# Performance work log

Measured on AMD Instinct MI355X. Metric: run time of the kernel, lower is better.

The kernel has to match this reference:

```python
import jax, jax.numpy as jnp
import numpy as np
import math

BLOCK = 256
NUM_HEADS = 32
HEAD_DIM = 128
HIDDEN = 2048
INNER = NUM_HEADS * HEAD_DIM
SEQ = 4096
EPS = 1e-5
LAYER_IDX = 0
NUM_LAYERS = 32


def _build_slopes(n):
    def get_slopes(n):
        def pow2(m):
            start = 2 ** (-2 ** (-(math.log2(m) - 3)))
            return [start * start ** i for i in range(m)]
        if math.log2(n).is_integer():
            return pow2(n)
        c = 2 ** math.floor(math.log2(n))
        return pow2(c) + get_slopes(2 * c)[0::2][: n - c]
    s = np.asarray(get_slopes(n), dtype=np.float32).reshape(n, 1, 1)
    # layer decay scaling as in __init__
    s = s * (1.0 - LAYER_IDX / (NUM_LAYERS - 1) + 1e-5)
    return s


def setup_inputs() -> dict:
    key = jax.random.key(0)
    k1, k2, k3, k4 = jax.random.split(key, 4)
    sd_h = 1.0 / math.sqrt(HIDDEN)
    sd_i = 1.0 / math.sqrt(INNER)
    return {
        "hidden_states": jax.random.normal(k1, (SEQ, HIDDEN), jnp.float32),
        "w_qkv": jax.random.normal(k2, (HIDDEN, 3 * INNER), jnp.float32) * sd_h,
        "w_gate": jax.random.normal(k3, (HIDDEN, INNER), jnp.float32) * sd_h,
        "w_out": jax.random.normal(k4, (INNER, HIDDEN), jnp.float32) * sd_i,
        "norm_weight": jnp.ones((INNER,), jnp.float32),
        "slope_rate": jnp.asarray(_build_slopes(NUM_HEADS)),
        "kv_cache": jnp.zeros((NUM_HEADS, HEAD_DIM, HEAD_DIM), jnp.float32),
    }


def _lightning_attention(q, k, v, slope, kv0):
    # q,k,v: [h, n, d]; slope: [h,1,1]; kv0: [h, d, d]
    h, n, d = q.shape
    nb = n // BLOCK
    qb = q.reshape(h, nb, BLOCK, d).transpose(1, 0, 2, 3)  # [nb,h,B,d]
    kb = k.reshape(h, nb, BLOCK, d).transpose(1, 0, 2, 3)
    vb = v.reshape(h, nb, BLOCK, d).transpose(1, 0, 2, 3)

    idx = jnp.arange(BLOCK, dtype=jnp.float32)
    diff = idx[:, None] - idx[None, :]                      # i - j
    s = slope.reshape(h, 1, 1)
    intra_decay = jnp.where(diff >= 0, jnp.exp(-s * diff), 0.0)   # [h,B,B]
    q_decay = jnp.exp(-s * (idx + 1.0).reshape(1, BLOCK, 1))      # [h,B,1]
    k_decay = jnp.exp(-s * (BLOCK - 1.0 - idx).reshape(1, BLOCK, 1))  # [h,B,1]
    block_decay = jnp.exp(-s * BLOCK)                             # [h,1,1]

    def step(kv, blk):
        qc, kc, vc = blk  # each [h,B,d]
        scores = jnp.einsum('hid,hjd->hij', qc, kc) * intra_decay
        o_intra = jnp.einsum('hij,hjd->hid', scores, vc)
        o_inter = q_decay * jnp.einsum('hid,hde->hie', qc, kv)
        kv_new = block_decay * kv + jnp.einsum('hjd,hje->hde', kc * k_decay, vc)
        return kv_new, o_intra + o_inter

    kv_final, outs = jax.lax.scan(step, kv0, (qb, kb, vb))
    out = outs.transpose(1, 0, 2, 3).reshape(h, n, d)
    return out, kv_final


def reference(hidden_states, w_qkv, w_gate, w_out, norm_weight, slope_rate, kv_cache):
    n = hidden_states.shape[0]
    # qkv projection + SiLU activation (done in fp32 in the original)
    qkv = jax.nn.silu(hidden_states @ w_qkv)                  # [n, 3*inner]
    qkv = qkv.reshape(n, NUM_HEADS, 3 * HEAD_DIM)
    q, k, v = jnp.split(qkv, 3, axis=-1)                      # [n,h,d] each
    q = q.transpose(1, 0, 2)                                  # [h,n,d]
    k = k.transpose(1, 0, 2)
    v = v.transpose(1, 0, 2)

    attn, kv_final = _lightning_attention(q, k, v, slope_rate, kv_cache)
    attn = attn.transpose(1, 0, 2).reshape(n, INNER)          # n (h d)

    # RMSNorm (fp32) then sigmoid gate then output projection
    var = jnp.mean(attn * attn, axis=-1, keepdims=True)
    normed = attn * jax.lax.rsqrt(var + EPS) * norm_weight
    gate = jax.nn.sigmoid(hidden_states @ w_gate)
    out = (gate * normed) @ w_out                             # [n, hidden]
    return out
```

## Files before the change

### kernel.cpp

```cpp
#include <hip/hip_runtime.h>
#include <stdint.h>

typedef __bf16 bf16x8 __attribute__((ext_vector_type(8)));
typedef float  f32x4  __attribute__((ext_vector_type(4)));
typedef unsigned short u16x8 __attribute__((ext_vector_type(8)));

__device__ __forceinline__ unsigned short f2bf(float f) {
    union { float f; uint32_t u; } x; x.f = f;
    uint32_t r = (x.u + 0x7FFFu + ((x.u >> 16) & 1u)) >> 16;
    return (unsigned short)r;
}
__device__ __forceinline__ float bf2f(unsigned short b) {
    union { uint32_t u; float f; } x; x.u = ((uint32_t)b) << 16;
    return x.f;
}

__device__ __forceinline__ void gl16(const void* g, void* l) {
    __builtin_amdgcn_global_load_lds(
        (const __attribute__((address_space(1))) void*)g,
        (__attribute__((address_space(3))) void*)(uint32_t)(uintptr_t)l,
        16, 0, 0);
}

#define MFMA16(a, b, c) __builtin_amdgcn_mfma_f32_16x16x32_bf16((a), (b), (c), 0, 0, 0)

__global__ __launch_bounds__(256) void f32_to_bf16_kernel(const float* __restrict__ in,
                                                          unsigned short* __restrict__ out,
                                                          int n8) {
    int i = blockIdx.x * 256 + threadIdx.x;
    if (i >= n8) return;
    float4 a = ((const float4*)in)[2 * i];
    float4 b = ((const float4*)in)[2 * i + 1];
    u16x8 o;
    o[0] = f2bf(a.x); o[1] = f2bf(a.y); o[2] = f2bf(a.z); o[3] = f2bf(a.w);
    o[4] = f2bf(b.x); o[5] = f2bf(b.y); o[6] = f2bf(b.z); o[7] = f2bf(b.w);
    ((u16x8*)out)[i] = o;
}

__global__ __launch_bounds__(256) void transpose_w_kernel(const float* __restrict__ in,
                                                          unsigned short* __restrict__ out,
                                                          int R, int C) {
    __shared__ float tile[32][33];
    int c0 = blockIdx.x * 32, r0 = blockIdx.y * 32;
    int lx = threadIdx.x & 31, ly = threadIdx.x >> 5;
#pragma unroll
    for (int i = ly; i < 32; i += 8)
        tile[i][lx] = in[(size_t)(r0 + i) * C + c0 + lx];
    __syncthreads();
#pragma unroll
    for (int i = ly; i < 32; i += 8)
        out[(size_t)(c0 + i) * R + r0 + lx] = f2bf(tile[lx][i]);
}

template <int ACT, int OUTF32>
__global__ __launch_bounds__(512, 2) void gemm256_kernel(const unsigned short* __restrict__ A,
                                                         const unsigned short* __restrict__ Bt,
                                                         void* __restrict__ Cout,
                                                         int N, int K, int NBN) {
    __shared__ unsigned short Abuf[2][2][8192];
    __shared__ unsigned short Bbuf[2][2][8192];

    int nwg = gridDim.x;
    int bid = blockIdx.x;
    int wg = (bid & 7) * (nwg >> 3) + (bid >> 3);
    int bm = wg / NBN, bn = wg % NBN;
    int tid = threadIdx.x, lane = tid & 63, w = tid >> 6;
    int wr = w >> 2, wc = w & 3;

    int r0 = tid >> 3;
    int cbs = (tid & 7) << 4;
    int el0 = (cbs ^ ((r0 & 7) << 4)) >> 1;
    int r1 = 64 + r0;
    int el1 = (cbs ^ ((r1 & 7) << 4)) >> 1;
    int lo0 = tid * 16, lo1 = 8192 + tid * 16;

    const unsigned short* Ag0 = A + (size_t)(bm * 256) * K;
    const unsigned short* Ag1 = A + (size_t)(bm * 256 + 128) * K;
    const unsigned short* Bg0 = Bt + (size_t)(bn * 256) * K;
    const unsigned short* Bg1 = Bt + (size_t)(bn * 256 + 128) * K;

#define STAGE(src, dstHalf, k0)                                            \
    do {                                                                   \
        gl16((src) + (size_t)r0 * K + (k0) + el0, (char*)(dstHalf) + lo0); \
        gl16((src) + (size_t)r1 * K + (k0) + el1, (char*)(dstHalf) + lo1); \
    } while (0)

    int aRow = wr * 64 + (lane & 15);
    int bRow = wc * 32 + (lane & 15);
    int swz = (lane & 7) << 4;
    int cbb = (lane >> 4) << 4;

#define RD_A(slot, R, m, kk) \
    af[R][m][kk] = *(const bf16x8*)((const char*)Abuf[slot][R] + ((aRow + (m) * 16) << 7) + (((kk) * 64 + cbb) ^ swz))
#define RD_B(slot, Cq, n, kk) \
    bfr[Cq][n][kk] = *(const bf16x8*)((const char*)Bbuf[slot][Cq] + ((bRow + (n) * 16) << 7) + (((kk) * 64 + cbb) ^ swz))

#define QUAD(q, Rh, Cc)                                                       \
    do {                                                                      \
        _Pragma("unroll")                                                     \
        for (int m = 0; m < 4; ++m)                                           \
            _Pragma("unroll")                                                 \
            for (int n = 0; n < 2; ++n) {                                     \
                acc[q][m][n] = MFMA16(af[Rh][m][0], bfr[Cc][n][0], acc[q][m][n]); \
                acc[q][m][n] = MFMA16(af[Rh][m][1], bfr[Cc][n][1], acc[q][m][n]); \
            }                                                                 \
    } while (0)

    bf16x8 af[2][4][2];
    bf16x8 bfr[2][2][2];
    f32x4 acc[4][4][2];
#pragma unroll
    for (int q = 0; q < 4; ++q)
#pragma unroll
        for (int m = 0; m < 4; ++m)
#pragma unroll
            for (int n = 0; n < 2; ++n)
#pragma unroll
                for (int r = 0; r < 4; ++r) acc[q][m][n][r] = 0.f;

    int NT = K >> 6;
    STAGE(Ag0, Abuf[0][0], 0);
    STAGE(Bg0, Bbuf[0][0], 0);
    STAGE(Ag1, Abuf[0][1], 0);
    STAGE(Bg1, Bbuf[0][1], 0);
    STAGE(Ag0, Abuf[1][0], 64);
    STAGE(Bg0, Bbuf[1][0], 64);
    STAGE(Ag1, Abuf[1][1], 64);
    STAGE(Bg1, Bbuf[1][1], 64);
    asm volatile("s_waitcnt vmcnt(8)" ::: "memory");
    __builtin_amdgcn_s_barrier();
#pragma unroll
    for (int m = 0; m < 4; ++m) { RD_A(0, 0, m, 0); RD_A(0, 0, m, 1); }
#pragma unroll
    for (int n = 0; n < 2; ++n) { RD_B(0, 0, n, 0); RD_B(0, 0, n, 1); }

    for (int t = 0; t < NT; ++t) {
        int cur = t & 1, nx = cur ^ 1;
        bool rd = (t + 1 < NT);
        bool st = (t + 2 < NT);
        int ks = (t + 2) << 6;

#pragma unroll
        for (int m = 0; m < 4; ++m) { RD_A(cur, 1, m, 0); RD_A(cur, 1, m, 1); }
        asm volatile("s_waitcnt lgkmcnt(8)" ::: "memory");
        __builtin_amdgcn_sched_barrier(0);
        __builtin_amdgcn_s_setprio(1);
        QUAD(0, 0, 0);
        __builtin_amdgcn_s_setprio(0);

#pragma unroll
        for (int n = 0; n < 2; ++n) { RD_B(cur, 1, n, 0); RD_B(cur, 1, n, 1); }
        asm volatile("s_waitcnt lgkmcnt(4)" ::: "memory");
        __builtin_amdgcn_sched_barrier(0);
        __builtin_amdgcn_s_setprio(1);
        QUAD(1, 1, 0);
        __builtin_amdgcn_s_setprio(0);

        asm volatile("s_waitcnt lgkmcnt(0)" ::: "memory");
        asm volatile("s_waitcnt vmcnt(0)" ::: "memory");
        __builtin_amdgcn_s_barrier();
        if (st) {
            STAGE(Ag0, Abuf[cur][0], ks);
            STAGE(Bg0, Bbuf[cur][0], ks);
        }
        if (rd) {
#pragma unroll
            for (int n = 0; n < 2; ++n) { RD_B(nx, 0, n, 0); RD_B(nx, 0, n, 1); }
        }
        __builtin_amdgcn_s_setprio(1);
        QUAD(2, 0, 1);
        __builtin_amdgcn_s_setprio(0);

        if (st) {
            STAGE(Ag1, Abuf[cur][1], ks);
            STAGE(Bg1, Bbuf[cur][1], ks);
        }
        if (rd) {
#pragma unroll
            for (int m = 0; m < 4; ++m) { RD_A(nx, 0, m, 0); RD_A(nx, 0, m, 1); }
        }
        __builtin_amdgcn_s_setprio(1);
        QUAD(3, 1, 1);
        __builtin_amdgcn_s_setprio(0);
    }

#pragma unroll
    for (int q = 0; q < 4; ++q) {
        const int R_ = q & 1, C_ = q >> 1;
#pragma unroll
        for (int m = 0; m < 4; ++m) {
            int row0 = bm * 256 + R_ * 128 + wr * 64 + m * 16 + ((lane >> 4) * 4);
#pragma unroll
            for (int n = 0; n < 2; ++n) {
                int col = bn * 256 + C_ * 128 + wc * 32 + n * 16 + (lane & 15);
#pragma unroll
                for (int rg = 0; rg < 4; ++rg) {
                    float v = acc[q][m][n][rg];
                    if (ACT == 1) v = v / (1.f + __expf(-v));
                    else if (ACT == 2) v = 1.f / (1.f + __expf(-v));
                    size_t idx = (size_t)(row0 + rg) * N + col;
                    if (OUTF32) ((float*)Cout)[idx] = v;
                    else        ((unsigned short*)Cout)[idx] = f2bf(v);
                }
            }
        }
    }
#undef STAGE
#undef RD_A
#undef RD_B
#undef QUAD
}

__global__ __launch_bounds__(256) void kv_transpose_kernel(const unsigned short* __restrict__ qkv,
                                                           const float* __restrict__ slopes,
                                                           unsigned short* __restrict__ kts,
                                                           unsigned short* __restrict__ vt) {
    __shared__ unsigned short tk[32][33];
    __shared__ unsigned short tv[32][33];
    int n0 = blockIdx.x * 32, d0 = blockIdx.y * 32, h = blockIdx.z;
    float s = slopes[h];
    int lx = threadIdx.x & 31, ly = threadIdx.x >> 5;
#pragma unroll
    for (int i = ly; i < 32; i += 8) {
        int n = n0 + i;
        size_t rowb = (size_t)n * 12288 + h * 384;
        float kv = bf2f(qkv[rowb + 128 + d0 + lx]) * __expf(-s * (float)(255 - (n & 255)));
        tk[i][lx] = f2bf(kv);
        tv[i][lx] = qkv[rowb + 256 + d0 + lx];
    }
    __syncthreads();
#pragma unroll
    for (int i = ly; i < 32; i += 8) {
        size_t ob = (size_t)(h * 128 + d0 + i) * 4096 + n0 + lx;
        kts[ob] = tk[lx][i];
        vt[ob] = tv[lx][i];
    }
}

__global__ __launch_bounds__(256) void kv_outer_kernel(const unsigned short* __restrict__ kts,
                                                       const unsigned short* __restrict__ vt,
                                                       float* __restrict__ U) {
    __shared__ unsigned short Kc[128 * 64];
    __shared__ unsigned short Vc[128 * 64];
    int blk = blockIdx.x;
    int h = blk & 31, t = blk >> 5;
    int tid = threadIdx.x, lane = tid & 63, w = tid >> 6;

    f32x4 acc[2][8];
#pragma unroll
    for (int m = 0; m < 2; ++m)
#pragma unroll
        for (int n = 0; n < 8; ++n)
#pragma unroll
            for (int r = 0; r < 4; ++r) acc[m][n][r] = 0.f;

    for (int ks = 0; ks < 4; ++ks) {
        __syncthreads();
#pragma unroll
        for (int it = 0; it < 4; ++it) {
            int slot = it * 256 + tid;
            int o = slot * 16;
            int r = o >> 7;
            int cb = o & 127;
            int scb = cb ^ ((r & 7) << 4);
            size_t j = (size_t)t * 256 + ks * 64 + (scb >> 1);
            gl16(kts + (size_t)(h * 128 + r) * 4096 + j, (char*)Kc + o);
            gl16(vt + (size_t)(h * 128 + r) * 4096 + j, (char*)Vc + o);
        }
        __syncthreads();
#pragma unroll
        for (int kk = 0; kk < 2; ++kk) {
            int kb = kk * 64 + ((lane >> 4) * 16);
            bf16x8 vf[2], kf[8];
#pragma unroll
            for (int m = 0; m < 2; ++m) {
                int e = w * 32 + m * 16 + (lane & 15);
                vf[m] = *(const bf16x8*)((const char*)Vc + (e << 7) + (kb ^ ((e & 7) << 4)));
            }
#pragma unroll
            for (int n = 0; n < 8; ++n) {
                int d = n * 16 + (lane & 15);
                kf[n] = *(const bf16x8*)((const char*)Kc + (d << 7) + (kb ^ ((d & 7) << 4)));
            }
#pragma unroll
            for (int m = 0; m < 2; ++m)
#pragma unroll
                for (int n = 0; n < 8; ++n)
                    acc[m][n] = MFMA16(vf[m], kf[n], acc[m][n]);
        }
    }
    size_t base = (size_t)(h * 16 + t) * 16384;
#pragma unroll
    for (int m = 0; m < 2; ++m)
#pragma unroll
        for (int n = 0; n < 8; ++n)
#pragma unroll
            for (int r = 0; r < 4; ++r) {
                int e = w * 32 + m * 16 + ((lane >> 4) * 4) + r;
                int d = n * 16 + (lane & 15);
                U[base + (size_t)e * 128 + d] = acc[m][n][r];
            }
}

__global__ __launch_bounds__(256) void kv_scan_kernel(const float* __restrict__ kv_cache,
                                                      const float* __restrict__ U,
                                                      const float* __restrict__ slopes,
                                                      unsigned short* __restrict__ Wb) {
    int h = blockIdx.x >> 3;
    int c0 = (blockIdx.x & 7) * 2048;
    int tid = threadIdx.x;
    float s = slopes[h];
    float bd = __expf(-s * 256.f);
    float wst[8];
    size_t hb = (size_t)h * 16384;
#pragma unroll
    for (int i = 0; i < 8; ++i) {
        int idx = c0 + i * 256 + tid;
        int e = idx >> 7, d = idx & 127;
        wst[i] = kv_cache[hb + (size_t)d * 128 + e];
    }
    for (int t = 0; t < 16; ++t) {
        size_t base = (size_t)(h * 16 + t) * 16384 + c0;
#pragma unroll
        for (int i = 0; i < 8; ++i) {
            int idx = i * 256 + tid;
            Wb[base + idx] = f2bf(wst[i]);
            wst[i] = bd * wst[i] + U[base + idx];
        }
    }
}

__global__ __launch_bounds__(256, 1) void attn_out_kernel(const unsigned short* __restrict__ qkv,
                                                          const unsigned short* __restrict__ vt,
                                                          const unsigned short* __restrict__ Wb,
                                                          const float* __restrict__ slopes,
                                                          unsigned short* __restrict__ attn) {
    __shared__ unsigned short lds[65536];
    unsigned short* Qs = lds;
    unsigned short* Ps = lds + 32768;
    unsigned short* KW = lds + 49152;
    unsigned short* Ks = KW;
    unsigned short* Vs = KW + 8192;

    int blk = blockIdx.x;
    int h = blk & 31, t = blk >> 5;
    float s = slopes[h];
    int tid = threadIdx.x, lane = tid & 63, w = tid >> 6;

#pragma unroll
    for (int it = 0; it < 16; ++it) {
        int slot = it * 256 + tid;
        int o = slot * 16;
        int r = o >> 8, cb = o & 255, scb = cb ^ ((r & 7) << 4);
        gl16(qkv + (size_t)(t * 256 + r) * 12288 + h * 384 + (scb >> 1), (char*)Qs + o);
    }
#pragma unroll
    for (int it = 0; it < 8; ++it) {
        int slot = it * 256 + tid;
        int o = slot * 16;
        int e = o >> 8, cb = o & 255, scb = cb ^ ((e & 7) << 4);
        gl16(Wb + (size_t)((h * 16 + t) * 128 + e) * 128 + (scb >> 1), (char*)KW + o);
    }
    __syncthreads();

    f32x4 acc[4][8];
#pragma unroll
    for (int m = 0; m < 4; ++m)
#pragma unroll
        for (int n = 0; n < 8; ++n)
#pragma unroll
            for (int r = 0; r < 4; ++r) acc[m][n][r] = 0.f;

#pragma unroll
    for (int kk = 0; kk < 4; ++kk) {
        int kb = kk * 64 + ((lane >> 4) * 16);
        bf16x8 qf[4], wf[8];
#pragma unroll
        for (int m = 0; m < 4; ++m) {
            int r = w * 64 + m * 16 + (lane & 15);
            qf[m] = *(const bf16x8*)((const char*)Qs + (r << 8) + (kb ^ ((r & 7) << 4)));
        }
#pragma unroll
        for (int n = 0; n < 8; ++n) {
            int e = n * 16 + (lane & 15);
            wf[n] = *(const bf16x8*)((const char*)KW + (e << 8) + (kb ^ ((e & 7) << 4)));
        }
#pragma unroll
        for (int m = 0; m < 4; ++m)
#pragma unroll
            for (int n = 0; n < 8; ++n)
                acc[m][n] = MFMA16(qf[m], wf[n], acc[m][n]);
    }
#pragma unroll
    for (int m = 0; m < 4; ++m)
#pragma unroll
        for (int rg = 0; rg < 4; ++rg) {
            int i = w * 64 + m * 16 + ((lane >> 4) * 4) + rg;
            float qd = __expf(-s * (float)(i + 1));
#pragma unroll
            for (int n = 0; n < 8; ++n) acc[m][n][rg] *= qd;
        }

    for (int jb = 0; jb < 4; ++jb) {
        __syncthreads();
#pragma unroll
        for (int it = 0; it < 4; ++it) {
            int slot = it * 256 + tid;
            int o = slot * 16;
            int r = o >> 8, cb = o & 255, scb = cb ^ ((r & 7) << 4);
            gl16(qkv + (size_t)(t * 256 + jb * 64 + r) * 12288 + h * 384 + 128 + (scb >> 1),
                 (char*)Ks + o);
        }
#pragma unroll
        for (int it = 0; it < 4; ++it) {
            int slot = it * 256 + tid;
            int o = slot * 16;
            int e = o >> 7, cb = o & 127, scb = cb ^ ((e & 7) << 4);
            gl16(vt + (size_t)(h * 128 + e) * 4096 + t * 256 + jb * 64 + (scb >> 1),
                 (char*)Vs + o);
        }
        __syncthreads();

        if (jb <= w) {
            f32x4 sc[4][4];
#pragma unroll
            for (int m = 0; m < 4; ++m)
#pragma unroll
                for (int n = 0; n < 4; ++n)
#pragma unroll
                    for (int r = 0; r < 4; ++r) sc[m][n][r] = 0.f;
#pragma unroll
            for (int kk = 0; kk < 4; ++kk) {
                int kb = kk * 64 + ((lane >> 4) * 16);
                bf16x8 qf[4], kf[4];
#pragma unroll
                for (int m = 0; m < 4; ++m) {
                    int r = w * 64 + m * 16 + (lane & 15);
                    qf[m] = *(const bf16x8*)((const char*)Qs + (r << 8) + (kb ^ ((r & 7) << 4)));
                }
#pragma unroll
                for (int n = 0; n < 4; ++n) {
                    int r = n * 16 + (lane & 15);
                    kf[n] = *(const bf16x8*)((const char*)Ks + (r << 8) + (kb ^ ((r & 7) << 4)));
                }
#pragma unroll
                for (int m = 0; m < 4; ++m)
#pragma unroll
                    for (int n = 0; n < 4; ++n)
                        sc[m][n] = MFMA16(qf[m], kf[n], sc[m][n]);
            }
            unsigned short* Pw = Ps + w * 4096;
#pragma unroll
            for (int m = 0; m < 4; ++m)
#pragma unroll
                for (int n = 0; n < 4; ++n)
#pragma unroll
                    for (int rg = 0; rg < 4; ++rg) {
                        int il = m * 16 + ((lane >> 4) * 4) + rg;
                        int i = w * 64 + il;
                        int jl = n * 16 + (lane & 15);
                        int j = jb * 64 + jl;
                        float v = 0.f;
                        if (i >= j) v = sc[m][n][rg] * __expf(-s * (float)(i - j));
                        int cb2 = (jl * 2) ^ ((il & 7) << 4);
                        *(unsigned short*)((char*)Pw + (il << 7) + cb2) = f2bf(v);
                    }
            asm volatile("s_waitcnt lgkmcnt(0)" ::: "memory");
#pragma unroll
            for (int kk = 0; kk < 2; ++kk) {
                int kb = kk * 64 + ((lane >> 4) * 16);
                bf16x8 pf[4], vf[8];
#pragma unroll
                for (int m = 0; m < 4; ++m) {
                    int il = m * 16 + (lane & 15);
                    pf[m] = *(const bf16x8*)((const char*)Pw + (il << 7) + (kb ^ ((il & 7) << 4)));
                }
#pragma unroll
                for (int n = 0; n < 8; ++n) {
                    int e = n * 16 + (lane & 15);
                    vf[n] = *(const bf16x8*)((const char*)Vs + (e << 7) + (kb ^ ((e & 7) << 4)));
                }
#pragma unroll
                for (int m = 0; m < 4; ++m)
#pragma unroll
                    for (int n = 0; n < 8; ++n)
                        acc[m][n] = MFMA16(pf[m], vf[n], acc[m][n]);
            }
        }
    }

#pragma unroll
    for (int m = 0; m < 4; ++m)
#pragma unroll
        for (int n = 0; n < 8; ++n)
#pragma unroll
            for (int rg = 0; rg < 4; ++rg) {
                int i = w * 64 + m * 16 + ((lane >> 4) * 4) + rg;
                int col = h * 128 + n * 16 + (lane & 15);
                attn[(size_t)(t * 256 + i) * 4096 + col] = f2bf(acc[m][n][rg]);
            }
}

__global__ __launch_bounds__(256) void rms_gate_kernel(const unsigned short* __restrict__ attn,
                                                       const unsigned short* __restrict__ gate,
                                                       const float* __restrict__ nw,
                                                       unsigned short* __restrict__ gated) {
    int row = blockIdx.x, tid = threadIdx.x;
    int lane = tid & 63, w = tid >> 6;
    const unsigned short* ar = attn + (size_t)row * 4096 + tid * 16;
    u16x8 a0 = *(const u16x8*)ar;
    u16x8 a1 = *(const u16x8*)(ar + 8);
    float v[16];
    float ss = 0.f;
#pragma unroll
    for (int j = 0; j < 8; ++j) { v[j] = bf2f(a0[j]); v[8 + j] = bf2f(a1[j]); }
#pragma unroll
    for (int j = 0; j < 16; ++j) ss += v[j] * v[j];
#pragma unroll
    for (int o = 32; o > 0; o >>= 1) ss += __shfl_xor(ss, o);
    __shared__ float red[4];
    if (lane == 0) red[w] = ss;
    __syncthreads();
    float tot = red[0] + red[1] + red[2] + red[3];
    float rs = rsqrtf(tot * (1.f / 4096.f) + 1e-5f);
    const unsigned short* gr = gate + (size_t)row * 4096 + tid * 16;
    u16x8 g0 = *(const u16x8*)gr;
    u16x8 g1 = *(const u16x8*)(gr + 8);
    const float* nwp = nw + tid * 16;
    u16x8 o0, o1;
#pragma unroll
    for (int j = 0; j < 8; ++j) {
        o0[j] = f2bf(v[j] * rs * nwp[j] * bf2f(g0[j]));
        o1[j] = f2bf(v[8 + j] * rs * nwp[8 + j] * bf2f(g1[j]));
    }
    unsigned short* gp = gated + (size_t)row * 4096 + tid * 16;
    *(u16x8*)gp = o0;
    *(u16x8*)(gp + 8) = o1;
}

extern "C" void kernel_launch(void* const* d_in, const int* in_sizes, int n_in,
                              void* d_out, int out_size, void* d_ws, size_t ws_size,
                              hipStream_t stream) {
    const float* hs       = (const float*)d_in[0];
    const float* w_qkv    = (const float*)d_in[1];
    const float* w_gate   = (const float*)d_in[2];
    const float* w_out    = (const float*)d_in[3];
    const float* nw       = (const float*)d_in[4];
    const float* slopes   = (const float*)d_in[5];
    const float* kv_cache = (const float*)d_in[6];
    float* out = (float*)d_out;
    char* ws = (char*)d_ws;

    unsigned short* hsb  = (unsigned short*)(ws + 0);
    unsigned short* wqt  = (unsigned short*)(ws + 16777216);
    unsigned short* wgt  = (unsigned short*)(ws + 67108864);
    unsigned short* wot  = (unsigned short*)(ws + 83886080);
    unsigned short* qkv  = (unsigned short*)(ws + 100663296);
    unsigned short* gate = (unsigned short*)(ws + 201326592);
    unsigned short* kts  = (unsigned short*)(ws + 234881024);
    unsigned short* vt   = (unsigned short*)(ws + 268435456);
    float*          U    = (float*)(ws + 301989888);
    unsigned short* Wb   = (unsigned short*)(ws + 335544320);
    unsigned short* attn  = wqt;
    unsigned short* gated = qkv;

    f32_to_bf16_kernel<<<4096, 256, 0, stream>>>(hs, hsb, 1048576);
    {
        dim3 g(384, 64);
        transpose_w_kernel<<<g, 256, 0, stream>>>(w_qkv, wqt, 2048, 12288);
    }
    {
        dim3 g(128, 64);
        transpose_w_kernel<<<g, 256, 0, stream>>>(w_gate, wgt, 2048, 4096);
    }
    {
        dim3 g(64, 128);
        transpose_w_kernel<<<g, 256, 0, stream>>>(w_out, wot, 4096, 2048);
    }
    gemm256_kernel<1, 0><<<768, 512, 0, stream>>>(hsb, wqt, qkv, 12288, 2048, 48);
    gemm256_kernel<2, 0><<<256, 512, 0, stream>>>(hsb, wgt, gate, 4096, 2048, 16);
    {
        dim3 g(128, 4, 32);
        kv_transpose_kernel<<<g, 256, 0, stream>>>(qkv, slopes, kts, vt);
    }
    kv_outer_kernel<<<512, 256, 0, stream>>>(kts, vt, U);
    kv_scan_kernel<<<256, 256, 0, stream>>>(kv_cache, U, slopes, Wb);
    attn_out_kernel<<<512, 256, 0, stream>>>(qkv, vt, Wb, slopes, attn);
    rms_gate_kernel<<<4096, 256, 0, stream>>>(attn, gate, nw, gated);
    gemm256_kernel<0, 1><<<128, 512, 0, stream>>>(gated, wot, out, 2048, 4096, 8);
}
```

Measured before the change: 567.1 us.

## Switch GEMM to 256x128 tiles with triple-buffered LDS pipeline

```diff
diff --git a/kernel.cpp b/kernel.cpp
--- a/kernel.cpp
+++ b/kernel.cpp
@@ -57,15 +57,15 @@
                                                          const unsigned short* __restrict__ Bt,
                                                          void* __restrict__ Cout,
                                                          int N, int K, int NBN) {
-    __shared__ unsigned short Abuf[2][2][8192];
-    __shared__ unsigned short Bbuf[2][2][8192];
+    __shared__ unsigned short Abuf[3][16384];
+    __shared__ unsigned short Bbuf[3][8192];
 
     int nwg = gridDim.x;
     int bid = blockIdx.x;
     int wg = (bid & 7) * (nwg >> 3) + (bid >> 3);
     int bm = wg / NBN, bn = wg % NBN;
     int tid = threadIdx.x, lane = tid & 63, w = tid >> 6;
-    int wr = w >> 2, wc = w & 3;
+    int wr = w >> 1, wc = w & 1;
 
     int r0 = tid >> 3;
     int cbs = (tid & 7) << 4;
@@ -76,139 +76,132 @@
 
     const unsigned short* Ag0 = A + (size_t)(bm * 256) * K;
     const unsigned short* Ag1 = A + (size_t)(bm * 256 + 128) * K;
-    const unsigned short* Bg0 = Bt + (size_t)(bn * 256) * K;
-    const unsigned short* Bg1 = Bt + (size_t)(bn * 256 + 128) * K;
-
-#define STAGE(src, dstHalf, k0)                                            \
-    do {                                                                   \
-        gl16((src) + (size_t)r0 * K + (k0) + el0, (char*)(dstHalf) + lo0); \
-        gl16((src) + (size_t)r1 * K + (k0) + el1, (char*)(dstHalf) + lo1); \
+    const unsigned short* Bg  = Bt + (size_t)(bn * 128) * K;
+
+#define STAGEH(src, dstBase, k0)                                            \
+    do {                                                                    \
+        gl16((src) + (size_t)r0 * K + (k0) + el0, (char*)(dstBase) + lo0);  \
+        gl16((src) + (size_t)r1 * K + (k0) + el1, (char*)(dstBase) + lo1);  \
     } while (0)
 
     int aRow = wr * 64 + (lane & 15);
-    int bRow = wc * 32 + (lane & 15);
+    int bRow = wc * 64 + (lane & 15);
     int swz = (lane & 7) << 4;
     int cbb = (lane >> 4) << 4;
 
-#define RD_A(slot, R, m, kk) \
-    af[R][m][kk] = *(const bf16x8*)((const char*)Abuf[slot][R] + ((aRow + (m) * 16) << 7) + (((kk) * 64 + cbb) ^ swz))
-#define RD_B(slot, Cq, n, kk) \
-    bfr[Cq][n][kk] = *(const bf16x8*)((const char*)Bbuf[slot][Cq] + ((bRow + (n) * 16) << 7) + (((kk) * 64 + cbb) ^ swz))
-
-#define QUAD(q, Rh, Cc)                                                       \
-    do {                                                                      \
-        _Pragma("unroll")                                                     \
-        for (int m = 0; m < 4; ++m)                                           \
-            _Pragma("unroll")                                                 \
-            for (int n = 0; n < 2; ++n) {                                     \
-                acc[q][m][n] = MFMA16(af[Rh][m][0], bfr[Cc][n][0], acc[q][m][n]); \
-                acc[q][m][n] = MFMA16(af[Rh][m][1], bfr[Cc][n][1], acc[q][m][n]); \
-            }                                                                 \
+#define RD_A(slot, m, kk) \
+    af[m][kk] = *(const bf16x8*)((const char*)Abuf[slot] + ((aRow + (m) * 16) << 7) + (((kk) * 64 + cbb) ^ swz))
+#define RD_B(slot, n, kk) \
+    bf[n][kk] = *(const bf16x8*)((const char*)Bbuf[slot] + ((bRow + (n) * 16) << 7) + (((kk) * 64 + cbb) ^ swz))
+
+#define QPAIR(m0, n0)                                                        \
+    do {                                                                     \
+        _Pragma("unroll")                                                    \
+        for (int m = m0; m < m0 + 2; ++m)                                    \
+            _Pragma("unroll")                                                \
+            for (int n = n0; n < n0 + 2; ++n) {                              \
+                acc[m][n] = MFMA16(af[m][0], bf[n][0], acc[m][n]);           \
+                acc[m][n] = MFMA16(af[m][1], bf[n][1], acc[m][n]);           \
+            }                                                                \
     } while (0)
 
-    bf16x8 af[2][4][2];
-    bf16x8 bfr[2][2][2];
-    f32x4 acc[4][4][2];
-#pragma unroll
-    for (int q = 0; q < 4; ++q)
-#pragma unroll
-        for (int m = 0; m < 4; ++m)
-#pragma unroll
-            for (int n = 0; n < 2; ++n)
-#pragma unroll
-                for (int r = 0; r < 4; ++r) acc[q][m][n][r] = 0.f;
+    bf16x8 af[4][2];
+    bf16x8 bf[4][2];
+    f32x4 acc[4][4];
+#pragma unroll
+    for (int m = 0; m < 4; ++m)
+#pragma unroll
+        for (int n = 0; n < 4; ++n)
+#pragma unroll
+            for (int r = 0; r < 4; ++r) acc[m][n][r] = 0.f;
 
     int NT = K >> 6;
-    STAGE(Ag0, Abuf[0][0], 0);
-    STAGE(Bg0, Bbuf[0][0], 0);
-    STAGE(Ag1, Abuf[0][1], 0);
-    STAGE(Bg1, Bbuf[0][1], 0);
-    STAGE(Ag0, Abuf[1][0], 64);
-    STAGE(Bg0, Bbuf[1][0], 64);
-    STAGE(Ag1, Abuf[1][1], 64);
-    STAGE(Bg1, Bbuf[1][1], 64);
-    asm volatile("s_waitcnt vmcnt(8)" ::: "memory");
+#pragma unroll
+    for (int p = 0; p < 3; ++p) {
+        STAGEH(Ag0, Abuf[p], p * 64);
+        STAGEH(Bg,  Bbuf[p], p * 64);
+        STAGEH(Ag1, (char*)Abuf[p] + 16384, p * 64);
+    }
+    asm volatile("s_waitcnt vmcnt(12)" ::: "memory");
     __builtin_amdgcn_s_barrier();
-#pragma unroll
-    for (int m = 0; m < 4; ++m) { RD_A(0, 0, m, 0); RD_A(0, 0, m, 1); }
-#pragma unroll
-    for (int n = 0; n < 2; ++n) { RD_B(0, 0, n, 0); RD_B(0, 0, n, 1); }
-
+    __builtin_amdgcn_sched_barrier(0);
+#pragma unroll
+    for (int m = 0; m < 2; ++m) { RD_A(0, m, 0); RD_A(0, m, 1); }
+#pragma unroll
+    for (int n = 0; n < 2; ++n) { RD_B(0, n, 0); RD_B(0, n, 1); }
+
+    int s = 0;
     for (int t = 0; t < NT; ++t) {
-        int cur = t & 1, nx = cur ^ 1;
+        int sn = (s + 1 == 3) ? 0 : s + 1;
         bool rd = (t + 1 < NT);
-        bool st = (t + 2 < NT);
-        int ks = (t + 2) << 6;
-
-#pragma unroll
-        for (int m = 0; m < 4; ++m) { RD_A(cur, 1, m, 0); RD_A(cur, 1, m, 1); }
-        asm volatile("s_waitcnt lgkmcnt(8)" ::: "memory");
-        __builtin_amdgcn_sched_barrier(0);
-        __builtin_amdgcn_s_setprio(1);
-        QUAD(0, 0, 0);
-        __builtin_amdgcn_s_setprio(0);
-
-#pragma unroll
-        for (int n = 0; n < 2; ++n) { RD_B(cur, 1, n, 0); RD_B(cur, 1, n, 1); }
+        bool st = (t + 3 < NT);
+        int ks = (t + 3) << 6;
+
+#pragma unroll
+        for (int m = 2; m < 4; ++m) { RD_A(s, m, 0); RD_A(s, m, 1); }
         asm volatile("s_waitcnt lgkmcnt(4)" ::: "memory");
         __builtin_amdgcn_sched_barrier(0);
         __builtin_amdgcn_s_setprio(1);
-        QUAD(1, 1, 0);
+        QPAIR(0, 0);
         __builtin_amdgcn_s_setprio(0);
 
+#pragma unroll
+        for (int n = 2; n < 4; ++n) { RD_B(s, n, 0); RD_B(s, n, 1); }
+        asm volatile("s_waitcnt lgkmcnt(4)" ::: "memory");
+        __builtin_amdgcn_sched_barrier(0);
+        __builtin_amdgcn_s_setprio(1);
+        QPAIR(2, 0);
+        __builtin_amdgcn_s_setprio(0);
+
         asm volatile("s_waitcnt lgkmcnt(0)" ::: "memory");
-        asm volatile("s_waitcnt vmcnt(0)" ::: "memory");
+        if (t + 2 < NT) asm volatile("s_waitcnt vmcnt(6)" ::: "memory");
+        else            asm volatile("s_waitcnt vmcnt(0)" ::: "memory");
         __builtin_amdgcn_s_barrier();
+        __builtin_amdgcn_sched_barrier(0);
         if (st) {
-            STAGE(Ag0, Abuf[cur][0], ks);
-            STAGE(Bg0, Bbuf[cur][0], ks);
+            STAGEH(Ag0, Abuf[s], ks);
+            STAGEH(Bg,  Bbuf[s], ks);
         }
         if (rd) {
 #pragma unroll
-            for (int n = 0; n < 2; ++n) { RD_B(nx, 0, n, 0); RD_B(nx, 0, n, 1); }
+            for (int n = 0; n < 2; ++n) { RD_B(sn, n, 0); RD_B(sn, n, 1); }
         }
         __builtin_amdgcn_s_setprio(1);
-        QUAD(2, 0, 1);
+        QPAIR(0, 2);
         __builtin_amdgcn_s_setprio(0);
 
-        if (st) {
-            STAGE(Ag1, Abuf[cur][1], ks);
-            STAGE(Bg1, Bbuf[cur][1], ks);
-        }
+        if (st) STAGEH(Ag1, (char*)Abuf[s] + 16384, ks);
         if (rd) {
 #pragma unroll
-            for (int m = 0; m < 4; ++m) { RD_A(nx, 0, m, 0); RD_A(nx, 0, m, 1); }
+            for (int m = 0; m < 2; ++m) { RD_A(sn, m, 0); RD_A(sn, m, 1); }
         }
         __builtin_amdgcn_s_setprio(1);
-        QUAD(3, 1, 1);
+        QPAIR(2, 2);
         __builtin_amdgcn_s_setprio(0);
-    }
-
-#pragma unroll
-    for (int q = 0; q < 4; ++q) {
-        const int R_ = q & 1, C_ = q >> 1;
-#pragma unroll
-        for (int m = 0; m < 4; ++m) {
-            int row0 = bm * 256 + R_ * 128 + wr * 64 + m * 16 + ((lane >> 4) * 4);
-#pragma unroll
-            for (int n = 0; n < 2; ++n) {
-                int col = bn * 256 + C_ * 128 + wc * 32 + n * 16 + (lane & 15);
-#pragma unroll
-                for (int rg = 0; rg < 4; ++rg) {
-                    float v = acc[q][m][n][rg];
-                    if (ACT == 1) v = v / (1.f + __expf(-v));
-                    else if (ACT == 2) v = 1.f / (1.f + __expf(-v));
-                    size_t idx = (size_t)(row0 + rg) * N + col;
-                    if (OUTF32) ((float*)Cout)[idx] = v;
-                    else        ((unsigned short*)Cout)[idx] = f2bf(v);
-                }
-            }
-        }
-    }
-#undef STAGE
+        s = sn;
+    }
+
+#pragma unroll
+    for (int m = 0; m < 4; ++m) {
+        int row0 = bm * 256 + wr * 64 + m * 16 + ((lane >> 4) * 4);
+#pragma unroll
+        for (int n = 0; n < 4; ++n) {
+            int col = bn * 128 + wc * 64 + n * 16 + (lane & 15);
+#pragma unroll
+            for (int rg = 0; rg < 4; ++rg) {
+                float v = acc[m][n][rg];
+                if (ACT == 1) v = v / (1.f + __expf(-v));
+                else if (ACT == 2) v = 1.f / (1.f + __expf(-v));
+                size_t idx = (size_t)(row0 + rg) * N + col;
+                if (OUTF32) ((float*)Cout)[idx] = v;
+                else        ((unsigned short*)Cout)[idx] = f2bf(v);
+            }
+        }
+    }
+#undef STAGEH
 #undef RD_A
 #undef RD_B
-#undef QUAD
+#undef QPAIR
 }
 
 __global__ __launch_bounds__(256) void kv_transpose_kernel(const unsigned short* __restrict__ qkv,
@@ -577,8 +570,8 @@
         dim3 g(64, 128);
         transpose_w_kernel<<<g, 256, 0, stream>>>(w_out, wot, 4096, 2048);
     }
-    gemm256_kernel<1, 0><<<768, 512, 0, stream>>>(hsb, wqt, qkv, 12288, 2048, 48);
-    gemm256_kernel<2, 0><<<256, 512, 0, stream>>>(hsb, wgt, gate, 4096, 2048, 16);
+    gemm256_kernel<1, 0><<<1536, 512, 0, stream>>>(hsb, wqt, qkv, 12288, 2048, 96);
+    gemm256_kernel<2, 0><<<512, 512, 0, stream>>>(hsb, wgt, gate, 4096, 2048, 32);
     {
         dim3 g(128, 4, 32);
         kv_transpose_kernel<<<g, 256, 0, stream>>>(qkv, slopes, kts, vt);
@@ -587,5 +580,5 @@
     kv_scan_kernel<<<256, 256, 0, stream>>>(kv_cache, U, slopes, Wb);
     attn_out_kernel<<<512, 256, 0, stream>>>(qkv, vt, Wb, slopes, attn);
     rms_gate_kernel<<<4096, 256, 0, stream>>>(attn, gate, nw, gated);
-    gemm256_kernel<0, 1><<<128, 512, 0, stream>>>(gated, wot, out, 2048, 4096, 8);
-}
+    gemm256_kernel<0, 1><<<256, 512, 0, stream>>>(gated, wot, out, 2048, 4096, 16);
+}
```

After: 575.5 us. About the same (+1.5%).
